# Optimization experiments

Measured on AMD Instinct MI355X. Metric: run time of the kernel, lower is better.

Reference implementation:

```python
import jax, jax.numpy as jnp
import numpy as np
import math

D_MODEL = 1024
N_HEADS = 16
D_HEAD = D_MODEL // N_HEADS


def setup_inputs() -> dict:
    key = jax.random.key(0)
    ks = jax.random.split(key, 5)
    B, T, C = 4, 2048, D_MODEL
    s = 1.0 / math.sqrt(C)
    return {
        "x": jax.random.normal(ks[0], (B, T, C), dtype=jnp.float32),
        "qkv_w": jax.random.normal(ks[1], (3 * C, C), dtype=jnp.float32) * s,
        "qkv_b": jnp.zeros((3 * C,), dtype=jnp.float32),
        "out_w": jax.random.normal(ks[2], (C, C), dtype=jnp.float32) * s,
        "out_b": jnp.zeros((C,), dtype=jnp.float32),
    }


def reference(x, qkv_w, qkv_b, out_w, out_b):
    B, T, C = x.shape
    H, Dh = N_HEADS, D_HEAD
    qkv = x @ qkv_w.T + qkv_b              # [B,T,3C] (torch Linear: x W^T + b)
    q, k, v = jnp.split(qkv, 3, axis=-1)
    # [B,T,C] -> [B,H,T,Dh]
    q = q.reshape(B, T, H, Dh).transpose(0, 2, 1, 3)
    k = k.reshape(B, T, H, Dh).transpose(0, 2, 1, 3)
    v = v.reshape(B, T, H, Dh).transpose(0, 2, 1, 3)
    att = jnp.einsum("bhqd,bhkd->bhqk", q, k) / math.sqrt(Dh)
    causal = jnp.tril(jnp.ones((T, T), dtype=bool))  # True = keep
    att = jnp.where(causal, att, -jnp.inf)
    att = jax.nn.softmax(att, axis=-1)
    y = jnp.einsum("bhqk,bhkd->bhqd", att, v)
    y = y.transpose(0, 2, 1, 3).reshape(B, T, C)
    return y @ out_w.T + out_b
```

## Files before the change

kernel.cpp:

```cpp
#include <hip/hip_runtime.h>

typedef __attribute__((ext_vector_type(4))) float f32x4;
typedef __attribute__((ext_vector_type(16))) float f32x16;
typedef __attribute__((ext_vector_type(8))) __bf16 bf16x8;
typedef __attribute__((ext_vector_type(4))) __bf16 bf16x4;
typedef __attribute__((ext_vector_type(2))) unsigned u32x2;

#define MFMA_B16(a,b,c) __builtin_amdgcn_mfma_f32_16x16x32_bf16((a),(b),(c),0,0,0)
#define MFMA32(a,b,c)  __builtin_amdgcn_mfma_f32_32x32x16_bf16((a),(b),(c),0,0,0)

static constexpr int T_LEN  = 2048;
static constexpr int C_DIM  = 1024;
static constexpr int H_NUM  = 16;
static constexpr int D_HEADc = 64;
static constexpr float Q_PRESCALE = 0.125f * 1.4426950408889634f;

__device__ __forceinline__ void async16(const void* g, void* l) {
  __builtin_amdgcn_global_load_lds(
      (const __attribute__((address_space(1))) unsigned int*)g,
      (__attribute__((address_space(3))) unsigned int*)l, 16, 0, 0);
}

__device__ __forceinline__ unsigned cvtpk(float lo, float hi) {
  unsigned r;
  asm("v_cvt_pk_bf16_f32 %0, %1, %2" : "=v"(r) : "v"(lo), "v"(hi));
  return r;
}

__global__ __launch_bounds__(256) void cvt3_kernel(const float* __restrict__ a, __bf16* __restrict__ da, int na,
                                                   const float* __restrict__ b, __bf16* __restrict__ db, int nb,
                                                   const float* __restrict__ c, __bf16* __restrict__ dc, int nc) {
  int i = blockIdx.x * 256 + threadIdx.x;
  const float* s;
  __bf16* d;
  long j;
  if (i < na) { s = a; d = da; j = i; }
  else if (i < na + nb) { s = b; d = db; j = i - na; }
  else if (i < na + nb + nc) { s = c; d = dc; j = i - na - nb; }
  else return;
  float4 f = reinterpret_cast<const float4*>(s)[j];
  bf16x4 o;
  o.x = (__bf16)f.x; o.y = (__bf16)f.y; o.z = (__bf16)f.z; o.w = (__bf16)f.w;
  reinterpret_cast<bf16x4*>(d)[j] = o;
}

__global__ __launch_bounds__(256) void gemm_qkv(const __bf16* __restrict__ A,
                                                const __bf16* __restrict__ W,
                                                const float* __restrict__ bias,
                                                __bf16* __restrict__ qb,
                                                __bf16* __restrict__ kb,
                                                __bf16* __restrict__ vb) {
  constexpr int K = 1024;
  __shared__ __bf16 As[2][128 * 64];
  __shared__ __bf16 Bs[2][128 * 64];
  const int tid = threadIdx.x;
  const int wid = tid >> 6, lane = tid & 63, l16 = lane & 15, lg = lane >> 4;
  const int r8 = lane >> 3, sl = lane & 7;
  const int r7 = l16 & 7;
  const int wm = wid >> 1, wn = wid & 1;
  const int m0 = blockIdx.x * 128;
  const int n0 = blockIdx.y * 128;

  f32x4 acc[4][4];
#pragma unroll
  for (int i = 0; i < 4; ++i)
#pragma unroll
    for (int j = 0; j < 4; ++j) acc[i][j] = f32x4{0.f, 0.f, 0.f, 0.f};

  auto stageg = [&](int buf, int k0) {
#pragma unroll
    for (int it = 0; it < 4; ++it) {
      int chunk = it * 4 + wid;
      int row = chunk * 8 + r8;
      int scol = ((sl ^ (row & 7)) << 3);
      async16(A + (long)(m0 + row) * K + k0 + scol, &As[buf][chunk * 512]);
      async16(W + (long)(n0 + row) * K + k0 + scol, &Bs[buf][chunk * 512]);
    }
  };

  stageg(0, 0);
  int cur = 0;
  for (int k0 = 0; k0 < K; k0 += 64) {
    if (k0 + 64 < K) {
      stageg(cur ^ 1, k0 + 64);
      asm volatile("s_waitcnt vmcnt(8)" ::: "memory");
    } else {
      asm volatile("s_waitcnt vmcnt(0)" ::: "memory");
    }
    __builtin_amdgcn_s_barrier();
#pragma unroll
    for (int kt = 0; kt < 2; ++kt) {
      const int sw = ((((kt << 2) | lg) ^ r7) << 3);
      bf16x8 af[4], bfv[4];
#pragma unroll
      for (int mi = 0; mi < 4; ++mi)
        af[mi] = *reinterpret_cast<const bf16x8*>(&As[cur][(wm * 64 + mi * 16 + l16) * 64 + sw]);
#pragma unroll
      for (int nt = 0; nt < 4; ++nt)
        bfv[nt] = *reinterpret_cast<const bf16x8*>(&Bs[cur][(wn * 64 + nt * 16 + l16) * 64 + sw]);
#pragma unroll
      for (int mi = 0; mi < 4; ++mi)
#pragma unroll
        for (int nt = 0; nt < 4; ++nt)
          acc[mi][nt] = MFMA_B16(af[mi], bfv[nt], acc[mi][nt]);
    }
    __builtin_amdgcn_s_barrier();
    cur ^= 1;
  }

  const int which = n0 >> 10;
  if (which == 0) {
#pragma unroll
    for (int mi = 0; mi < 4; ++mi)
#pragma unroll
      for (int nt = 0; nt < 4; ++nt)
#pragma unroll
        for (int r = 0; r < 4; ++r) {
          int m = m0 + wm * 64 + mi * 16 + lg * 4 + r;
          int n = n0 + wn * 64 + nt * 16 + l16;
          int cc = n & 1023;
          int h = cc >> 6, d = cc & 63;
          long b = m >> 11, t = m & 2047;
          qb[(((b * H_NUM + h) * T_LEN) + t) * D_HEADc + d] =
              (__bf16)((acc[mi][nt][r] + bias[n]) * Q_PRESCALE);
        }
  } else if (which == 1) {
#pragma unroll
    for (int mi = 0; mi < 4; ++mi)
#pragma unroll
      for (int nt = 0; nt < 4; ++nt)
#pragma unroll
        for (int r = 0; r < 4; ++r) {
          int m = m0 + wm * 64 + mi * 16 + lg * 4 + r;
          int n = n0 + wn * 64 + nt * 16 + l16;
          int cc = n & 1023;
          int h = cc >> 6, d = cc & 63;
          long b = m >> 11, t = m & 2047;
          kb[(((b * H_NUM + h) * T_LEN) + t) * D_HEADc + d] = (__bf16)(acc[mi][nt][r] + bias[n]);
        }
  } else {
#pragma unroll
    for (int mi = 0; mi < 4; ++mi)
#pragma unroll
      for (int nt = 0; nt < 4; ++nt) {
        int n = n0 + wn * 64 + nt * 16 + l16;
        int cc = n & 1023;
        int h = cc >> 6, d = cc & 63;
        int t0 = m0 + wm * 64 + mi * 16 + lg * 4;
        long b = t0 >> 11;
        long t = t0 & 2047;
        float bv = bias[n];
        bf16x4 pk;
#pragma unroll
        for (int r = 0; r < 4; ++r) pk[r] = (__bf16)(acc[mi][nt][r] + bv);
        *reinterpret_cast<bf16x4*>(
            &vb[(((b * H_NUM + h) * D_HEADc) + d) * T_LEN + t]) = pk;
      }
  }
}

__global__ __launch_bounds__(512, 4) void attn_kernel(const __bf16* __restrict__ q,
                                                      const __bf16* __restrict__ k,
                                                      const __bf16* __restrict__ vt,
                                                      __bf16* __restrict__ y) {
  __shared__ __bf16 Ks[2][2][64 * 64];
  __shared__ __bf16 Vs[2][2][64 * 64];
  const int tid = threadIdx.x;
  const int wid = tid >> 6, lane = tid & 63;
  const int l31 = lane & 31, hi = lane >> 5;
  const int r8 = lane >> 3, sl = lane & 7;
  const int r7 = l31 & 7;
  const int bid = blockIdx.x;
  const int qt = 15 - (bid >> 6);
  const int bh = bid & 63;
  const int grp = wid >> 2;
  const int wq = wid & 3;
  const int q0 = qt * 128;
  const int qw = q0 + wq * 32;
  const int qglob = qw + l31;
  const __bf16* qg = q + (long)bh * T_LEN * D_HEADc;
  const __bf16* kg = k + (long)bh * T_LEN * D_HEADc;
  const __bf16* vg = vt + (long)bh * T_LEN * D_HEADc;
  const long bb = bh >> 4;
  const int h = bh & 15;

  union { unsigned short us[8]; bf16x8 v; } ones_u;
#pragma unroll
  for (int i = 0; i < 8; ++i) ones_u.us[i] = 0x3F80;
  const bf16x8 ones = ones_u.v;

  f32x16 z16;
#pragma unroll
  for (int r = 0; r < 16; ++r) z16[r] = 0.f;

  bf16x8 qf[4];
#pragma unroll
  for (int dt = 0; dt < 4; ++dt)
    qf[dt] = *reinterpret_cast<const bf16x8*>(qg + (long)qglob * D_HEADc + dt * 16 + hi * 8);

  f32x16 o[2];
  o[0] = z16; o[1] = z16;
  f32x16 lacc = z16;

  auto stage = [&](int buf, int i) {
#pragma unroll
    for (int it = 0; it < 4; ++it) {
      int slot = it * 8 + wid;
      int g = slot & 7;
      int kind = slot >> 3;
      int par = kind >> 1, isv = kind & 1;
      int row = g * 8 + r8;
      int scol = ((sl ^ (row & 7)) << 3);
      int k0s = (2 * i + par) * 64;
      if (!isv)
        async16(kg + (long)(k0s + row) * D_HEADc + scol, &Ks[buf][par][g * 512]);
      else
        async16(vg + (long)row * T_LEN + k0s + scol, &Vs[buf][par][g * 512]);
    }
  };

  const int iters = qt + 1;
  stage(0, 0);
  int cur = 0;
  for (int i = 0; i < iters; ++i) {
    if (i + 1 < iters) {
      stage(cur ^ 1, i + 1);
      asm volatile("s_waitcnt vmcnt(4)" ::: "memory");
    } else {
      asm volatile("s_waitcnt vmcnt(0)" ::: "memory");
    }
    __builtin_amdgcn_s_barrier();
    const int k0 = (2 * i + grp) * 64;
    if (k0 < qw + 32) {
      const __bf16* Kc = Ks[cur][grp];
      const __bf16* Vc = Vs[cur][grp];
      f32x16 s[2];
      __builtin_amdgcn_s_setprio(1);
      {
        const int swz = (hi ^ r7) << 3;
        bf16x8 kf0 = *reinterpret_cast<const bf16x8*>(&Kc[l31 * 64 + swz]);
        bf16x8 kf1 = *reinterpret_cast<const bf16x8*>(&Kc[(32 + l31) * 64 + swz]);
        s[0] = MFMA32(kf0, qf[0], z16);
        s[1] = MFMA32(kf1, qf[0], z16);
      }
#pragma unroll
      for (int dt = 1; dt < 4; ++dt) {
        const int swz = (((dt << 1) | hi) ^ r7) << 3;
        bf16x8 kf0 = *reinterpret_cast<const bf16x8*>(&Kc[l31 * 64 + swz]);
        bf16x8 kf1 = *reinterpret_cast<const bf16x8*>(&Kc[(32 + l31) * 64 + swz]);
        s[0] = MFMA32(kf0, qf[dt], s[0]);
        s[1] = MFMA32(kf1, qf[dt], s[1]);
      }
      __builtin_amdgcn_s_setprio(0);

      if (k0 + 63 > qw) {
#pragma unroll
        for (int r = 0; r < 16; ++r) {
          const int kb = (r & 3) + 8 * (r >> 2) + 4 * hi;
          if (k0 + kb > qglob) s[0][r] = -3e38f;
          if (k0 + 32 + kb > qglob) s[1][r] = -3e38f;
        }
      }

#pragma unroll
      for (int ki = 0; ki < 2; ++ki)
#pragma unroll
        for (int r = 0; r < 16; ++r) s[ki][r] = exp2f(s[ki][r]);

      unsigned pb[4][4];
#pragma unroll
      for (int ki = 0; ki < 2; ++ki) {
        unsigned d0 = cvtpk(s[ki][0], s[ki][1]),   d1 = cvtpk(s[ki][2], s[ki][3]);
        unsigned d2 = cvtpk(s[ki][4], s[ki][5]),   d3 = cvtpk(s[ki][6], s[ki][7]);
        unsigned d4 = cvtpk(s[ki][8], s[ki][9]),   d5 = cvtpk(s[ki][10], s[ki][11]);
        unsigned d6 = cvtpk(s[ki][12], s[ki][13]), d7 = cvtpk(s[ki][14], s[ki][15]);
        u32x2 a2 = __builtin_amdgcn_permlane32_swap(d0, d2, false, false);
        u32x2 b2 = __builtin_amdgcn_permlane32_swap(d1, d3, false, false);
        pb[ki * 2][0] = a2[0]; pb[ki * 2][1] = b2[0];
        pb[ki * 2][2] = a2[1]; pb[ki * 2][3] = b2[1];
        u32x2 c2 = __builtin_amdgcn_permlane32_swap(d4, d6, false, false);
        u32x2 e2 = __builtin_amdgcn_permlane32_swap(d5, d7, false, false);
        pb[ki * 2 + 1][0] = c2[0]; pb[ki * 2 + 1][1] = e2[0];
        pb[ki * 2 + 1][2] = c2[1]; pb[ki * 2 + 1][3] = e2[1];
      }

      __builtin_amdgcn_s_setprio(1);
#pragma unroll
      for (int kt = 0; kt < 4; ++kt) {
        union { unsigned u[4]; bf16x8 v; } pu;
#pragma unroll
        for (int w = 0; w < 4; ++w) pu.u[w] = pb[kt][w];
        const int swz = (((kt << 1) | hi) ^ r7) << 3;
        bf16x8 vf0 = *reinterpret_cast<const bf16x8*>(&Vc[l31 * 64 + swz]);
        bf16x8 vf1 = *reinterpret_cast<const bf16x8*>(&Vc[(32 + l31) * 64 + swz]);
        o[0] = MFMA32(vf0, pu.v, o[0]);
        o[1] = MFMA32(vf1, pu.v, o[1]);
        lacc = MFMA32(ones, pu.v, lacc);
      }
      __builtin_amdgcn_s_setprio(0);
    }
    __builtin_amdgcn_s_barrier();
    cur ^= 1;
  }

  float* ob  = (float*)&Ks[0][0][0];
  float* lb  = (float*)&Vs[0][0][0];
  if (grp == 1) {
#pragma unroll
    for (int di = 0; di < 2; ++di)
#pragma unroll
      for (int r = 0; r < 16; ++r) {
        const int kb = (r & 3) + 8 * (r >> 2) + 4 * hi;
        ob[wq * 2048 + (di * 32 + kb) * 32 + l31] = o[di][r];
      }
    if (hi == 0) lb[wq * 32 + l31] = lacc[0];
  }
  __syncthreads();
  if (grp == 0) {
    const float inv = 1.f / (lacc[0] + lb[wq * 32 + l31]);
    const long row = bb * T_LEN + qglob;
#pragma unroll
    for (int di = 0; di < 2; ++di)
#pragma unroll
      for (int rr = 0; rr < 4; ++rr) {
        bf16x4 pk;
#pragma unroll
        for (int c = 0; c < 4; ++c) {
          const int r = rr * 4 + c;
          const int kb = rr * 8 + hi * 4 + c;
          float val = o[di][r] + ob[wq * 2048 + (di * 32 + kb) * 32 + l31];
          pk[c] = (__bf16)(val * inv);
        }
        *reinterpret_cast<bf16x4*>(
            &y[row * C_DIM + h * D_HEADc + di * 32 + rr * 8 + hi * 4]) = pk;
      }
  }
}

__global__ __launch_bounds__(256) void gemm_proj(const __bf16* __restrict__ A,
                                                 const __bf16* __restrict__ W,
                                                 const float* __restrict__ bias,
                                                 float* __restrict__ out) {
  constexpr int K = 1024;
  __shared__ __bf16 As[2][128 * 64];
  __shared__ __bf16 Bs[2][128 * 64];
  const int tid = threadIdx.x;
  const int wid = tid >> 6, lane = tid & 63, l16 = lane & 15, lg = lane >> 4;
  const int r8 = lane >> 3, sl = lane & 7;
  const int r7 = l16 & 7;
  const int wm = wid >> 1, wn = wid & 1;
  const int m0 = blockIdx.x * 128, n0 = blockIdx.y * 128;

  f32x4 acc[4][4];
#pragma unroll
  for (int i = 0; i < 4; ++i)
#pragma unroll
    for (int j = 0; j < 4; ++j) acc[i][j] = f32x4{0.f, 0.f, 0.f, 0.f};

  auto stageg = [&](int buf, int k0) {
#pragma unroll
    for (int it = 0; it < 4; ++it) {
      int chunk = it * 4 + wid;
      int row = chunk * 8 + r8;
      int scol = ((sl ^ (row & 7)) << 3);
      async16(A + (long)(m0 + row) * K + k0 + scol, &As[buf][chunk * 512]);
      async16(W + (long)(n0 + row) * K + k0 + scol, &Bs[buf][chunk * 512]);
    }
  };

  stageg(0, 0);
  int cur = 0;
  for (int k0 = 0; k0 < K; k0 += 64) {
    if (k0 + 64 < K) {
      stageg(cur ^ 1, k0 + 64);
      asm volatile("s_waitcnt vmcnt(8)" ::: "memory");
    } else {
      asm volatile("s_waitcnt vmcnt(0)" ::: "memory");
    }
    __builtin_amdgcn_s_barrier();
#pragma unroll
    for (int kt = 0; kt < 2; ++kt) {
      const int sw = ((((kt << 2) | lg) ^ r7) << 3);
      bf16x8 af[4], bfv[4];
#pragma unroll
      for (int mi = 0; mi < 4; ++mi)
        af[mi] = *reinterpret_cast<const bf16x8*>(&As[cur][(wm * 64 + mi * 16 + l16) * 64 + sw]);
#pragma unroll
      for (int nt = 0; nt < 4; ++nt)
        bfv[nt] = *reinterpret_cast<const bf16x8*>(&Bs[cur][(wn * 64 + nt * 16 + l16) * 64 + sw]);
#pragma unroll
      for (int mi = 0; mi < 4; ++mi)
#pragma unroll
        for (int nt = 0; nt < 4; ++nt)
          acc[mi][nt] = MFMA_B16(af[mi], bfv[nt], acc[mi][nt]);
    }
    __builtin_amdgcn_s_barrier();
    cur ^= 1;
  }
#pragma unroll
  for (int mi = 0; mi < 4; ++mi)
#pragma unroll
    for (int nt = 0; nt < 4; ++nt)
#pragma unroll
      for (int r = 0; r < 4; ++r) {
        long m = m0 + wm * 64 + mi * 16 + lg * 4 + r;
        int n = n0 + wn * 64 + nt * 16 + l16;
        out[m * C_DIM + n] = acc[mi][nt][r] + bias[n];
      }
}

extern "C" void kernel_launch(void* const* d_in, const int* in_sizes, int n_in,
                              void* d_out, int out_size, void* d_ws, size_t ws_size,
                              hipStream_t stream) {
  const float* x     = (const float*)d_in[0];
  const float* qkv_w = (const float*)d_in[1];
  const float* qkv_b = (const float*)d_in[2];
  const float* out_w = (const float*)d_in[3];
  const float* out_b = (const float*)d_in[4];
  float* out = (float*)d_out;

  const long NX  = 8192L * 1024;
  const long NWQ = 3072L * 1024;
  const long NWO = 1024L * 1024;
  const size_t need = (size_t)(5 * NX + NWQ + NWO) * 2;
  if (ws_size < need) return;

  __bf16* xb   = (__bf16*)d_ws;
  __bf16* wqkv = xb + NX;
  __bf16* wout = wqkv + NWQ;
  __bf16* qb   = wout + NWO;
  __bf16* kb   = qb + NX;
  __bf16* vb   = kb + NX;
  __bf16* yb   = vb + NX;

  const int na = (int)(NX / 4), nb = (int)(NWQ / 4), nc = (int)(NWO / 4);
  cvt3_kernel<<<(na + nb + nc + 255) / 256, 256, 0, stream>>>(x, xb, na, qkv_w, wqkv, nb, out_w, wout, nc);

  gemm_qkv<<<dim3(64, 24), 256, 0, stream>>>(xb, wqkv, qkv_b, qb, kb, vb);
  attn_kernel<<<dim3(1024), 512, 0, stream>>>(qb, kb, vb, yb);
  gemm_proj<<<dim3(64, 8), 256, 0, stream>>>(yb, wout, out_b, out);
}
```

Baseline: 166.6 us.

## Give each attention wave its own query rows instead of splitting keys across groups

The attention kernel previously ran two 4-wave groups that each handled alternate 64-key tiles for the same 128 query rows, then merged their partial outputs through LDS. Now each of the 8 waves owns 32 distinct query rows of a 256-row tile and walks all keys, with 128-key K/V tiles staged per iteration. This removes the cross-group reduction and sync, and halves the grid to 512 blocks, reordered to pair heavy and light causal tiles. The trade-off is fewer blocks, more per-wave causal imbalance inside a block, and longer serial key loops.

```diff
diff --git a/kernel.cpp b/kernel.cpp
--- a/kernel.cpp
+++ b/kernel.cpp
@@ -163,20 +163,18 @@
                                                       const __bf16* __restrict__ k,
                                                       const __bf16* __restrict__ vt,
                                                       __bf16* __restrict__ y) {
-  __shared__ __bf16 Ks[2][2][64 * 64];
-  __shared__ __bf16 Vs[2][2][64 * 64];
+  __shared__ __bf16 Ks[2][128 * 64];
+  __shared__ __bf16 Vs[2][64 * 128];
   const int tid = threadIdx.x;
   const int wid = tid >> 6, lane = tid & 63;
   const int l31 = lane & 31, hi = lane >> 5;
-  const int r8 = lane >> 3, sl = lane & 7;
   const int r7 = l31 & 7;
   const int bid = blockIdx.x;
-  const int qt = 15 - (bid >> 6);
+  const int g = bid >> 6;
+  const int qt = (g < 4) ? (7 - g) : (g - 4);
   const int bh = bid & 63;
-  const int grp = wid >> 2;
-  const int wq = wid & 3;
-  const int q0 = qt * 128;
-  const int qw = q0 + wq * 32;
+  const int q0 = qt * 256;
+  const int qw = q0 + wid * 32;
   const int qglob = qw + l31;
   const __bf16* qg = q + (long)bh * T_LEN * D_HEADc;
   const __bf16* kg = k + (long)bh * T_LEN * D_HEADc;
@@ -203,23 +201,24 @@
   f32x16 lacc = z16;
 
   auto stage = [&](int buf, int i) {
-#pragma unroll
-    for (int it = 0; it < 4; ++it) {
-      int slot = it * 8 + wid;
-      int g = slot & 7;
-      int kind = slot >> 3;
-      int par = kind >> 1, isv = kind & 1;
-      int row = g * 8 + r8;
-      int scol = ((sl ^ (row & 7)) << 3);
-      int k0s = (2 * i + par) * 64;
-      if (!isv)
-        async16(kg + (long)(k0s + row) * D_HEADc + scol, &Ks[buf][par][g * 512]);
-      else
-        async16(vg + (long)row * T_LEN + k0s + scol, &Vs[buf][par][g * 512]);
+    const int kbase = i * 128;
+#pragma unroll
+    for (int r = 0; r < 2; ++r) {
+      int idx = r * 512 + tid;
+      int row = idx >> 3, c8 = idx & 7;
+      int scol = ((c8 ^ (row & 7)) << 3);
+      async16(kg + (long)(kbase + row) * D_HEADc + scol, &Ks[buf][idx * 8]);
+    }
+#pragma unroll
+    for (int r = 0; r < 2; ++r) {
+      int idx = r * 512 + tid;
+      int d = idx >> 4, c8 = idx & 15;
+      int scol = ((c8 ^ (d & 7)) << 3);
+      async16(vg + (long)d * T_LEN + kbase + scol, &Vs[buf][idx * 8]);
     }
   };
 
-  const int iters = qt + 1;
+  const int iters = 2 * (qt + 1);
   stage(0, 0);
   int cur = 0;
   for (int i = 0; i < iters; ++i) {
@@ -230,111 +229,93 @@
       asm volatile("s_waitcnt vmcnt(0)" ::: "memory");
     }
     __builtin_amdgcn_s_barrier();
-    const int k0 = (2 * i + grp) * 64;
-    if (k0 < qw + 32) {
-      const __bf16* Kc = Ks[cur][grp];
-      const __bf16* Vc = Vs[cur][grp];
-      f32x16 s[2];
-      __builtin_amdgcn_s_setprio(1);
-      {
-        const int swz = (hi ^ r7) << 3;
-        bf16x8 kf0 = *reinterpret_cast<const bf16x8*>(&Kc[l31 * 64 + swz]);
-        bf16x8 kf1 = *reinterpret_cast<const bf16x8*>(&Kc[(32 + l31) * 64 + swz]);
-        s[0] = MFMA32(kf0, qf[0], z16);
-        s[1] = MFMA32(kf1, qf[0], z16);
+#pragma unroll
+    for (int sub = 0; sub < 2; ++sub) {
+      const int k0 = i * 128 + sub * 64;
+      if (k0 < qw + 32) {
+        const __bf16* Kc = &Ks[cur][sub * 64 * 64];
+        f32x16 s[2];
+        __builtin_amdgcn_s_setprio(1);
+        {
+          const int swz = (hi ^ r7) << 3;
+          bf16x8 kf0 = *reinterpret_cast<const bf16x8*>(&Kc[l31 * 64 + swz]);
+          bf16x8 kf1 = *reinterpret_cast<const bf16x8*>(&Kc[(32 + l31) * 64 + swz]);
+          s[0] = MFMA32(kf0, qf[0], z16);
+          s[1] = MFMA32(kf1, qf[0], z16);
+        }
+#pragma unroll
+        for (int dt = 1; dt < 4; ++dt) {
+          const int swz = (((dt << 1) | hi) ^ r7) << 3;
+          bf16x8 kf0 = *reinterpret_cast<const bf16x8*>(&Kc[l31 * 64 + swz]);
+          bf16x8 kf1 = *reinterpret_cast<const bf16x8*>(&Kc[(32 + l31) * 64 + swz]);
+          s[0] = MFMA32(kf0, qf[dt], s[0]);
+          s[1] = MFMA32(kf1, qf[dt], s[1]);
+        }
+        __builtin_amdgcn_s_setprio(0);
+
+        if (k0 + 63 > qw) {
+#pragma unroll
+          for (int r = 0; r < 16; ++r) {
+            const int kb = (r & 3) + 8 * (r >> 2) + 4 * hi;
+            if (k0 + kb > qglob) s[0][r] = -3e38f;
+            if (k0 + 32 + kb > qglob) s[1][r] = -3e38f;
+          }
+        }
+
+#pragma unroll
+        for (int ki = 0; ki < 2; ++ki)
+#pragma unroll
+          for (int r = 0; r < 16; ++r) s[ki][r] = exp2f(s[ki][r]);
+
+        unsigned pb[4][4];
+#pragma unroll
+        for (int ki = 0; ki < 2; ++ki) {
+          unsigned d0 = cvtpk(s[ki][0], s[ki][1]),   d1 = cvtpk(s[ki][2], s[ki][3]);
+          unsigned d2 = cvtpk(s[ki][4], s[ki][5]),   d3 = cvtpk(s[ki][6], s[ki][7]);
+          unsigned d4 = cvtpk(s[ki][8], s[ki][9]),   d5 = cvtpk(s[ki][10], s[ki][11]);
+          unsigned d6 = cvtpk(s[ki][12], s[ki][13]), d7 = cvtpk(s[ki][14], s[ki][15]);
+          u32x2 a2 = __builtin_amdgcn_permlane32_swap(d0, d2, false, false);
+          u32x2 b2 = __builtin_amdgcn_permlane32_swap(d1, d3, false, false);
+          pb[ki * 2][0] = a2[0]; pb[ki * 2][1] = b2[0];
+          pb[ki * 2][2] = a2[1]; pb[ki * 2][3] = b2[1];
+          u32x2 c2 = __builtin_amdgcn_permlane32_swap(d4, d6, false, false);
+          u32x2 e2 = __builtin_amdgcn_permlane32_swap(d5, d7, false, false);
+          pb[ki * 2 + 1][0] = c2[0]; pb[ki * 2 + 1][1] = e2[0];
+          pb[ki * 2 + 1][2] = c2[1]; pb[ki * 2 + 1][3] = e2[1];
+        }
+
+        __builtin_amdgcn_s_setprio(1);
+#pragma unroll
+        for (int kt = 0; kt < 4; ++kt) {
+          union { unsigned u[4]; bf16x8 v; } pu;
+#pragma unroll
+          for (int w = 0; w < 4; ++w) pu.u[w] = pb[kt][w];
+          const int ch = (((sub << 3) | (kt << 1) | hi) ^ r7) << 3;
+          bf16x8 vf0 = *reinterpret_cast<const bf16x8*>(&Vs[cur][l31 * 128 + ch]);
+          bf16x8 vf1 = *reinterpret_cast<const bf16x8*>(&Vs[cur][(32 + l31) * 128 + ch]);
+          o[0] = MFMA32(vf0, pu.v, o[0]);
+          o[1] = MFMA32(vf1, pu.v, o[1]);
+          lacc = MFMA32(ones, pu.v, lacc);
+        }
+        __builtin_amdgcn_s_setprio(0);
       }
-#pragma unroll
-      for (int dt = 1; dt < 4; ++dt) {
-        const int swz = (((dt << 1) | hi) ^ r7) << 3;
-        bf16x8 kf0 = *reinterpret_cast<const bf16x8*>(&Kc[l31 * 64 + swz]);
-        bf16x8 kf1 = *reinterpret_cast<const bf16x8*>(&Kc[(32 + l31) * 64 + swz]);
-        s[0] = MFMA32(kf0, qf[dt], s[0]);
-        s[1] = MFMA32(kf1, qf[dt], s[1]);
-      }
-      __builtin_amdgcn_s_setprio(0);
-
-      if (k0 + 63 > qw) {
-#pragma unroll
-        for (int r = 0; r < 16; ++r) {
-          const int kb = (r & 3) + 8 * (r >> 2) + 4 * hi;
-          if (k0 + kb > qglob) s[0][r] = -3e38f;
-          if (k0 + 32 + kb > qglob) s[1][r] = -3e38f;
-        }
-      }
-
-#pragma unroll
-      for (int ki = 0; ki < 2; ++ki)
-#pragma unroll
-        for (int r = 0; r < 16; ++r) s[ki][r] = exp2f(s[ki][r]);
-
-      unsigned pb[4][4];
-#pragma unroll
-      for (int ki = 0; ki < 2; ++ki) {
-        unsigned d0 = cvtpk(s[ki][0], s[ki][1]),   d1 = cvtpk(s[ki][2], s[ki][3]);
-        unsigned d2 = cvtpk(s[ki][4], s[ki][5]),   d3 = cvtpk(s[ki][6], s[ki][7]);
-        unsigned d4 = cvtpk(s[ki][8], s[ki][9]),   d5 = cvtpk(s[ki][10], s[ki][11]);
-        unsigned d6 = cvtpk(s[ki][12], s[ki][13]), d7 = cvtpk(s[ki][14], s[ki][15]);
-        u32x2 a2 = __builtin_amdgcn_permlane32_swap(d0, d2, false, false);
-        u32x2 b2 = __builtin_amdgcn_permlane32_swap(d1, d3, false, false);
-        pb[ki * 2][0] = a2[0]; pb[ki * 2][1] = b2[0];
-        pb[ki * 2][2] = a2[1]; pb[ki * 2][3] = b2[1];
-        u32x2 c2 = __builtin_amdgcn_permlane32_swap(d4, d6, false, false);
-        u32x2 e2 = __builtin_amdgcn_permlane32_swap(d5, d7, false, false);
-        pb[ki * 2 + 1][0] = c2[0]; pb[ki * 2 + 1][1] = e2[0];
-        pb[ki * 2 + 1][2] = c2[1]; pb[ki * 2 + 1][3] = e2[1];
-      }
-
-      __builtin_amdgcn_s_setprio(1);
-#pragma unroll
-      for (int kt = 0; kt < 4; ++kt) {
-        union { unsigned u[4]; bf16x8 v; } pu;
-#pragma unroll
-        for (int w = 0; w < 4; ++w) pu.u[w] = pb[kt][w];
-        const int swz = (((kt << 1) | hi) ^ r7) << 3;
-        bf16x8 vf0 = *reinterpret_cast<const bf16x8*>(&Vc[l31 * 64 + swz]);
-        bf16x8 vf1 = *reinterpret_cast<const bf16x8*>(&Vc[(32 + l31) * 64 + swz]);
-        o[0] = MFMA32(vf0, pu.v, o[0]);
-        o[1] = MFMA32(vf1, pu.v, o[1]);
-        lacc = MFMA32(ones, pu.v, lacc);
-      }
-      __builtin_amdgcn_s_setprio(0);
     }
     __builtin_amdgcn_s_barrier();
     cur ^= 1;
   }
 
-  float* ob  = (float*)&Ks[0][0][0];
-  float* lb  = (float*)&Vs[0][0][0];
-  if (grp == 1) {
-#pragma unroll
-    for (int di = 0; di < 2; ++di)
-#pragma unroll
-      for (int r = 0; r < 16; ++r) {
-        const int kb = (r & 3) + 8 * (r >> 2) + 4 * hi;
-        ob[wq * 2048 + (di * 32 + kb) * 32 + l31] = o[di][r];
-      }
-    if (hi == 0) lb[wq * 32 + l31] = lacc[0];
-  }
-  __syncthreads();
-  if (grp == 0) {
-    const float inv = 1.f / (lacc[0] + lb[wq * 32 + l31]);
-    const long row = bb * T_LEN + qglob;
-#pragma unroll
-    for (int di = 0; di < 2; ++di)
-#pragma unroll
-      for (int rr = 0; rr < 4; ++rr) {
-        bf16x4 pk;
-#pragma unroll
-        for (int c = 0; c < 4; ++c) {
-          const int r = rr * 4 + c;
-          const int kb = rr * 8 + hi * 4 + c;
-          float val = o[di][r] + ob[wq * 2048 + (di * 32 + kb) * 32 + l31];
-          pk[c] = (__bf16)(val * inv);
-        }
-        *reinterpret_cast<bf16x4*>(
-            &y[row * C_DIM + h * D_HEADc + di * 32 + rr * 8 + hi * 4]) = pk;
-      }
-  }
+  const float inv = 1.f / lacc[0];
+  const long row = bb * T_LEN + qglob;
+#pragma unroll
+  for (int di = 0; di < 2; ++di)
+#pragma unroll
+    for (int rr = 0; rr < 4; ++rr) {
+      bf16x4 pk;
+#pragma unroll
+      for (int c = 0; c < 4; ++c) pk[c] = (__bf16)(o[di][rr * 4 + c] * inv);
+      *reinterpret_cast<bf16x4*>(
+          &y[row * C_DIM + h * D_HEADc + di * 32 + rr * 8 + hi * 4]) = pk;
+    }
 }
 
 __global__ __launch_bounds__(256) void gemm_proj(const __bf16* __restrict__ A,
@@ -437,6 +418,6 @@
   cvt3_kernel<<<(na + nb + nc + 255) / 256, 256, 0, stream>>>(x, xb, na, qkv_w, wqkv, nb, out_w, wout, nc);
 
   gemm_qkv<<<dim3(64, 24), 256, 0, stream>>>(xb, wqkv, qkv_b, qb, kb, vb);
-  attn_kernel<<<dim3(1024), 512, 0, stream>>>(qb, kb, vb, yb);
+  attn_kernel<<<dim3(512), 512, 0, stream>>>(qb, kb, vb, yb);
   gemm_proj<<<dim3(64, 8), 256, 0, stream>>>(yb, wout, out_b, out);
 }
```

After: 185.4 us. +11.3%, slower.

## Single-buffer V tiles in attention to cut LDS and raise occupancy

Applied to the files above, without the earlier changes.

The attention kernel keeps double-buffered K tiles but loads V into a single LDS buffer at the start of each iteration. A second wait and barrier are added between the QK/softmax phase and the PV phase, so the V load overlaps with the score computation. This cuts shared memory per block from 64KB to 48KB, allowing more resident blocks per CU, and the launch-bounds minimum blocks is raised to match. In exchange, V load latency is hidden only behind QK^T work, each iteration pays an extra barrier, and the tighter register budget may cause spills.

```diff
diff --git a/kernel.cpp b/kernel.cpp
--- a/kernel.cpp
+++ b/kernel.cpp
@@ -159,12 +159,12 @@
   }
 }
 
-__global__ __launch_bounds__(512, 4) void attn_kernel(const __bf16* __restrict__ q,
+__global__ __launch_bounds__(512, 6) void attn_kernel(const __bf16* __restrict__ q,
                                                       const __bf16* __restrict__ k,
                                                       const __bf16* __restrict__ vt,
                                                       __bf16* __restrict__ y) {
   __shared__ __bf16 Ks[2][2][64 * 64];
-  __shared__ __bf16 Vs[2][2][64 * 64];
+  __shared__ __bf16 Vs[2][64 * 64];
   const int tid = threadIdx.x;
   const int wid = tid >> 6, lane = tid & 63;
   const int l31 = lane & 31, hi = lane >> 5;
@@ -202,38 +202,46 @@
   o[0] = z16; o[1] = z16;
   f32x16 lacc = z16;
 
-  auto stage = [&](int buf, int i) {
-#pragma unroll
-    for (int it = 0; it < 4; ++it) {
+  auto stageK = [&](int buf, int i) {
+#pragma unroll
+    for (int it = 0; it < 2; ++it) {
       int slot = it * 8 + wid;
-      int g = slot & 7;
-      int kind = slot >> 3;
-      int par = kind >> 1, isv = kind & 1;
+      int par = slot >> 3, g = slot & 7;
       int row = g * 8 + r8;
       int scol = ((sl ^ (row & 7)) << 3);
       int k0s = (2 * i + par) * 64;
-      if (!isv)
-        async16(kg + (long)(k0s + row) * D_HEADc + scol, &Ks[buf][par][g * 512]);
-      else
-        async16(vg + (long)row * T_LEN + k0s + scol, &Vs[buf][par][g * 512]);
+      async16(kg + (long)(k0s + row) * D_HEADc + scol, &Ks[buf][par][g * 512]);
     }
   };
+  auto stageV = [&](int i) {
+#pragma unroll
+    for (int it = 0; it < 2; ++it) {
+      int slot = it * 8 + wid;
+      int par = slot >> 3, g = slot & 7;
+      int row = g * 8 + r8;
+      int scol = ((sl ^ (row & 7)) << 3);
+      int k0s = (2 * i + par) * 64;
+      async16(vg + (long)row * T_LEN + k0s + scol, &Vs[par][g * 512]);
+    }
+  };
 
   const int iters = qt + 1;
-  stage(0, 0);
+  stageK(0, 0);
   int cur = 0;
   for (int i = 0; i < iters; ++i) {
+    stageV(i);
     if (i + 1 < iters) {
-      stage(cur ^ 1, i + 1);
+      stageK(cur ^ 1, i + 1);
       asm volatile("s_waitcnt vmcnt(4)" ::: "memory");
     } else {
-      asm volatile("s_waitcnt vmcnt(0)" ::: "memory");
+      asm volatile("s_waitcnt vmcnt(2)" ::: "memory");
     }
     __builtin_amdgcn_s_barrier();
     const int k0 = (2 * i + grp) * 64;
-    if (k0 < qw + 32) {
+    const bool active = (k0 < qw + 32);
+    unsigned pb[4][4];
+    if (active) {
       const __bf16* Kc = Ks[cur][grp];
-      const __bf16* Vc = Vs[cur][grp];
       f32x16 s[2];
       __builtin_amdgcn_s_setprio(1);
       {
@@ -267,7 +275,6 @@
 #pragma unroll
         for (int r = 0; r < 16; ++r) s[ki][r] = exp2f(s[ki][r]);
 
-      unsigned pb[4][4];
 #pragma unroll
       for (int ki = 0; ki < 2; ++ki) {
         unsigned d0 = cvtpk(s[ki][0], s[ki][1]),   d1 = cvtpk(s[ki][2], s[ki][3]);
@@ -283,7 +290,17 @@
         pb[ki * 2 + 1][0] = c2[0]; pb[ki * 2 + 1][1] = e2[0];
         pb[ki * 2 + 1][2] = c2[1]; pb[ki * 2 + 1][3] = e2[1];
       }
-
+    }
+
+    if (i + 1 < iters) {
+      asm volatile("s_waitcnt vmcnt(2)" ::: "memory");
+    } else {
+      asm volatile("s_waitcnt vmcnt(0)" ::: "memory");
+    }
+    __builtin_amdgcn_s_barrier();
+
+    if (active) {
+      const __bf16* Vc = Vs[grp];
       __builtin_amdgcn_s_setprio(1);
 #pragma unroll
       for (int kt = 0; kt < 4; ++kt) {
@@ -304,7 +321,7 @@
   }
 
   float* ob  = (float*)&Ks[0][0][0];
-  float* lb  = (float*)&Vs[0][0][0];
+  float* lb  = (float*)&Vs[0][0];
   if (grp == 1) {
 #pragma unroll
     for (int di = 0; di < 2; ++di)
```

New measurement: 434.7 us. 2.61x slower.
